# Kernel optimization log

Hardware: AMD Instinct MI355X
Metric: run time of the kernel (lower is better)

Reference implementation:

```python
import jax, jax.numpy as jnp
import numpy as np

NUM_PROPOSALS = 200000
NUM_OBJECTS = 128
N_CLS = 256
POS_THR = 0.4
NEG_THR = 0.1
REG_FACTOR = 10.0


def _make_boxes(key, n, img=1000.0, max_wh=200.0):
    k1, k2 = jax.random.split(key)
    xy = jax.random.uniform(k1, (n, 2), jnp.float32) * (img - max_wh)
    wh = jax.random.uniform(k2, (n, 2), jnp.float32) * (max_wh - 1.0) + 1.0
    return jnp.concatenate([xy, xy + wh], axis=-1)  # valid xyxy boxes


def setup_inputs() -> dict:
    key = jax.random.key(0)
    k1, k2, k3 = jax.random.split(key, 3)
    return {
        "objectness_score": jax.random.normal(k1, (NUM_PROPOSALS,), jnp.float32),
        "proposals": _make_boxes(k2, NUM_PROPOSALS),
        "gt_bounding_box": _make_boxes(k3, NUM_OBJECTS)[None],  # (1, N, 4)
    }


def _box_iou(b1, b2):
    # b1: (N,4), b2: (M,4) in xyxy -> (N, M)
    a1 = (b1[:, 2] - b1[:, 0]) * (b1[:, 3] - b1[:, 1])
    a2 = (b2[:, 2] - b2[:, 0]) * (b2[:, 3] - b2[:, 1])
    lt = jnp.maximum(b1[:, None, :2], b2[None, :, :2])
    rb = jnp.minimum(b1[:, None, 2:], b2[None, :, 2:])
    wh = jnp.clip(rb - lt, 0.0)
    inter = wh[..., 0] * wh[..., 1]
    return inter / (a1[:, None] + a2[None, :] - inter)


def _rpn_loss(objectness_score, proposals, gt_bounding_box):
    gt = gt_bounding_box[0]                      # (N, 4)
    iou = _box_iou(gt, proposals)                # (N, M)
    N, M = iou.shape
    flat = iou.reshape(-1)                       # (N*M,)

    # top-N best (gt, proposal) pairs, indices only (non-differentiable path)
    _, best_idx = jax.lax.top_k(flat, N)

    key = jax.random.key(42)
    k1, k2, k3 = jax.random.split(key, 3)
    neg_inf = jnp.float32(-jnp.inf)

    # random-priority sampling == randperm + truncate over candidate multiset
    pos_prio = jnp.where(flat > POS_THR, jax.random.uniform(k1, (N * M,)), neg_inf)
    best_prio = jax.random.uniform(k2, (N,))
    cand_prio = jnp.concatenate([best_prio, pos_prio])
    cand_idx = jnp.concatenate([best_idx, jnp.arange(N * M)])

    num_pos = N_CLS // 2   # always filled: best_idx contributes N=128 candidates
    num_neg = N_CLS - num_pos

    sel_p, loc = jax.lax.top_k(cand_prio, num_pos)
    pos_flat = cand_idx[loc]
    pos_valid = jnp.isfinite(sel_p)
    pos_rows = pos_flat // M
    pos_cols = pos_flat % M

    neg_prio = jnp.where(flat < NEG_THR, jax.random.uniform(k3, (N * M,)), neg_inf)
    sel_n, neg_flat = jax.lax.top_k(neg_prio, num_neg)
    neg_valid = jnp.isfinite(sel_n)
    neg_cols = neg_flat % M

    # classification: BCE-with-logits, mean over valid samples
    logits = jnp.concatenate([objectness_score[pos_cols], objectness_score[neg_cols]])
    labels = jnp.concatenate([jnp.ones((num_pos,), jnp.float32), jnp.zeros((num_neg,), jnp.float32)])
    w = jnp.concatenate([pos_valid, neg_valid]).astype(jnp.float32)
    bce = jnp.maximum(logits, 0.0) - logits * labels + jnp.log1p(jnp.exp(-jnp.abs(logits)))
    cls_loss = jnp.sum(bce * w) / jnp.maximum(jnp.sum(w), 1.0)

    d = proposals[pos_cols] - gt[pos_rows]       # (num_pos, 4)
    ad = jnp.abs(d)
    sl1 = jnp.where(ad < 1.0, 0.5 * d * d, ad - 0.5)
    wp = pos_valid.astype(jnp.float32)[:, None]
    reg_loss = jnp.sum(sl1 * wp) / jnp.maximum(jnp.sum(wp) * 4.0, 1.0)

    return cls_loss + REG_FACTOR * reg_loss


def reference(objectness_score, proposals, gt_bounding_box):
    return _rpn_loss(objectness_score, proposals, gt_bounding_box)
```

## Files before the change

### kernel.cpp

```cpp
#include <hip/hip_runtime.h>
#include <stdint.h>

#pragma clang fp contract(off)

typedef unsigned long long u64;
typedef uint32_t u32;

#define M_PROP 200000u
#define N_GT   128u
#define NM     25600000u
#define GSPLIT 4u
#define GPART  32u

#define BCUT 8355840u
#define CCUT 8387584u
#define IB_POS 0x3ECCCCCDu

#define SHARDS 16u
#define SHARD_CAP 4096u
#define ACAP_SHARD 65536u
#define TOPA_CAP 8192u
#define COMP_CAP 8192u
#define ACAP_L 512u

#define CSLOT(i) counters[(u32)(i) * 256u]

__host__ __device__ inline void tf2x32(u32 k0, u32 k1, u32 x0, u32 x1,
                                       u32& o0, u32& o1) {
  u32 ks0 = k0, ks1 = k1, ks2 = k0 ^ k1 ^ 0x1BD11BDAu;
  x0 += ks0; x1 += ks1;
#define TF_R(r) { x0 += x1; x1 = (x1 << r) | (x1 >> (32 - r)); x1 ^= x0; }
  TF_R(13) TF_R(15) TF_R(26) TF_R(6)
  x0 += ks1; x1 += ks2 + 1u;
  TF_R(17) TF_R(29) TF_R(16) TF_R(24)
  x0 += ks2; x1 += ks0 + 2u;
  TF_R(13) TF_R(15) TF_R(26) TF_R(6)
  x0 += ks0; x1 += ks1 + 3u;
  TF_R(17) TF_R(29) TF_R(16) TF_R(24)
  x0 += ks1; x1 += ks2 + 4u;
  TF_R(13) TF_R(15) TF_R(26) TF_R(6)
  x0 += ks2; x1 += ks0 + 5u;
#undef TF_R
  o0 = x0; o1 = x1;
}

__device__ inline u32 jax_bits32(u32 ka, u32 kb, u32 idx) {
  u32 a, b; tf2x32(ka, kb, 0u, idx, a, b);
  return a ^ b;
}

static void jax_split3(u32& k1a, u32& k1b, u32& k2a, u32& k2b,
                       u32& k3a, u32& k3b) {
  const u32 K0 = 0u, K1 = 42u;
  tf2x32(K0, K1, 0u, 0u, k1a, k1b);
  tf2x32(K0, K1, 0u, 1u, k2a, k2b);
  tf2x32(K0, K1, 0u, 2u, k3a, k3b);
}

__device__ inline u32 wave_append_slot(u32* ctr, bool pred, bool& any) {
  u64 mask = __ballot(pred);
  if (mask == 0ull) { any = false; return 0u; }
  any = true;
  u32 lane = threadIdx.x & 63u;
  u32 prefix = (u32)__popcll(mask & ((1ull << lane) - 1ull));
  int leader = __ffsll(mask) - 1;
  u32 base = 0u;
  if ((int)lane == leader) base = atomicAdd(ctr, (u32)__popcll(mask));
  base = __shfl(base, leader, 64);
  return base + prefix;
}

__device__ inline void wave_append4(u32* ctr, u64* buf, u32 cap,
                                    const bool* p, const u64* v) {
  u64 m0 = __ballot(p[0]);
  u64 m1 = __ballot(p[1]);
  u64 m2 = __ballot(p[2]);
  u64 m3 = __ballot(p[3]);
  u32 lane = threadIdx.x & 63u;
  u64 laneLT = (1ull << lane) - 1ull;
  u32 n0 = (u32)__popcll(m0), n1 = (u32)__popcll(m1);
  u32 n2 = (u32)__popcll(m2), n3 = (u32)__popcll(m3);
  int leader = __ffsll(m0 | m1 | m2 | m3) - 1;
  u32 base = 0u;
  if ((int)lane == leader) base = atomicAdd(ctr, n0 + n1 + n2 + n3);
  base = __shfl(base, leader, 64);
  if (p[0]) { u32 s = base + (u32)__popcll(m0 & laneLT); if (s < cap) buf[s] = v[0]; }
  base += n0;
  if (p[1]) { u32 s = base + (u32)__popcll(m1 & laneLT); if (s < cap) buf[s] = v[1]; }
  base += n1;
  if (p[2]) { u32 s = base + (u32)__popcll(m2 & laneLT); if (s < cap) buf[s] = v[2]; }
  base += n2;
  if (p[3]) { u32 s = base + (u32)__popcll(m3 & laneLT); if (s < cap) buf[s] = v[3]; }
}

__device__ inline u32 iouBin(u32 bits) {
  u32 b = (bits - 0x3E800000u) >> 14;
  return b > 1023u ? 1023u : b;
}

__global__ __launch_bounds__(256) void rpn_collect(
    const float4* __restrict__ props, const float4* __restrict__ gt,
    u64* __restrict__ bufA, u64* __restrict__ bufB, u64* __restrict__ bufC,
    u32* __restrict__ counters, u32* __restrict__ gHistA,
    u32 k1a, u32 k1b, u32 k3a, u32 k3b) {
  __shared__ float4 gtS[GPART];
  __shared__ float gtAreaS[GPART];
  __shared__ u32 hA[1024];
  __shared__ u64 listA[4][ACAP_L];
  const u32 tid = threadIdx.x;
  const u32 lane = tid & 63u;
  const u32 wid = tid >> 6;
  const u32 gbase = blockIdx.y * GPART;
  for (u32 i = tid; i < 1024u; i += 256u) hA[i] = 0u;
  for (u32 j = tid; j < GPART; j += 256u) {
    float4 gb = gt[gbase + j];
    gtS[j] = gb;
    gtAreaS[j] = (gb.z - gb.x) * (gb.w - gb.y);
  }
  __syncthreads();

  const u32 shard = (blockIdx.x * GSPLIT + blockIdx.y) & (SHARDS - 1u);
  u32* cntC_g = &CSLOT(shard);
  u32* cntB_g = &CSLOT(16u + shard);
  u32* cntA_g = &CSLOT(32u + shard);
  u64* myBufC = bufC + (size_t)shard * SHARD_CAP;
  u64* myBufB = bufB + (size_t)shard * SHARD_CAP;
  u64* myBufA = bufA + (size_t)shard * ACAP_SHARD;

  u32 p = blockIdx.x * 256u + tid;
  bool active = p < M_PROP;
  float4 pb = make_float4(0.f, 0.f, 0.f, 0.f);
  if (active) pb = props[p];
  float pa = (pb.z - pb.x) * (pb.w - pb.y);

  u32 cntA = 0u;
  const u64 laneLT = (1ull << lane) - 1ull;

#define PROCESS_A()                                                          \
  {                                                                          \
    for (u32 i = lane; i < cntA; i += 64u) {                                 \
      u64 kv = listA[wid][i];                                                \
      bool anyk;                                                             \
      u32 sk = wave_append_slot(cntA_g, true, anyk);                         \
      if (sk < ACAP_SHARD) myBufA[sk] = kv;                                  \
      u32 ib = (u32)(kv >> 25);                                              \
      u32 bidx = 0x1FFFFFFu - (u32)(kv & 0x1FFFFFFu);                        \
      u32 m1 = jax_bits32(k1a, k1b, bidx) >> 9;                              \
      bool keep = (ib > IB_POS) && (m1 >= BCUT);                             \
      bool anyb;                                                             \
      u32 sb2 = wave_append_slot(cntB_g, keep, anyb);                        \
      if (keep && sb2 < SHARD_CAP)                                           \
        myBufB[sb2] = ((u64)m1 << 25) | (u64)(0x1FFFFFFu - (bidx + 128u));   \
    }                                                                        \
    cntA = 0u;                                                               \
  }

  u32 idxRun = gbase * M_PROP + p;
  for (u32 gg = 0u; gg < GPART; gg += 4u) {
    float iou[4]; u32 ib[4], idx[4], m3[4];
    bool aa[4], cc[4];
#pragma unroll
    for (u32 r = 0u; r < 4u; ++r) {
      float4 gb = gtS[gg + r];
      float ga = gtAreaS[gg + r];
      float wx = fminf(gb.z, pb.z) - fmaxf(gb.x, pb.x);
      float wy = fminf(gb.w, pb.w) - fmaxf(gb.y, pb.y);
      wx = fmaxf(wx, 0.0f); wy = fmaxf(wy, 0.0f);
      float inter = wx * wy;
      iou[r] = inter / (ga + pa - inter);
      ib[r] = __float_as_uint(iou[r]);
      idx[r] = idxRun; idxRun += M_PROP;
      m3[r] = jax_bits32(k3a, k3b, idx[r]) >> 9;
      aa[r] = active && (iou[r] > 0.25f);
      cc[r] = active && (iou[r] < 0.1f) && (m3[r] >= CCUT);
      if (aa[r]) atomicAdd(&hA[iouBin(ib[r])], 1u);
    }
#pragma unroll
    for (u32 r = 0u; r < 4u; ++r) {
      u64 ma = __ballot(aa[r]);
      if (ma) {
        u32 pfx = (u32)__popcll(ma & laneLT);
        if (aa[r])
          listA[wid][cntA + pfx] = ((u64)ib[r] << 25) | (u64)(0x1FFFFFFu - idx[r]);
        cntA += (u32)__popcll(ma);
      }
    }
    u64 mc = __ballot(cc[0] | cc[1] | cc[2] | cc[3]);
    if (mc) {
      u64 cv[4];
#pragma unroll
      for (u32 r = 0u; r < 4u; ++r)
        cv[r] = ((u64)m3[r] << 25) | (u64)(0x1FFFFFFu - idx[r]);
      wave_append4(cntC_g, myBufC, SHARD_CAP, cc, cv);
    }
    if (cntA > ACAP_L - 256u) PROCESS_A();
  }
  PROCESS_A();
#undef PROCESS_A

  __syncthreads();
  for (u32 b = tid; b < 1024u; b += 256u) {
    u32 v = hA[b];
    if (v) atomicAdd(&gHistA[b], v);
  }
}

__global__ __launch_bounds__(256) void rpn_filterA(
    const u64* __restrict__ bufA, const u32* __restrict__ gHistA,
    u32* __restrict__ counters, u64* __restrict__ bufTopA) {
  const u32 tid = threadIdx.x;
  const u32 lane = tid & 63u;
  u32 loc[16]; u32 t = 0u;
  const u32 bbase = lane * 16u;
#pragma unroll
  for (u32 j = 0u; j < 16u; ++j) { loc[j] = gHistA[bbase + j]; t += loc[j]; }
  u32 suf = t;
  for (u32 off = 1u; off < 64u; off <<= 1u) {
    u32 o = __shfl_down(suf, off, 64);
    if (lane + off < 64u) suf += o;
  }
  u32 cum = suf - t;
  u32 cand = 0u; bool found = false;
#pragma unroll
  for (int j = 15; j >= 0; --j) {
    cum += loc[j];
    if (!found && cum >= 128u) { cand = bbase + (u32)j; found = true; }
  }
  for (u32 off = 1u; off < 64u; off <<= 1u) {
    u32 o = __shfl_xor(cand, off, 64);
    cand = o > cand ? o : cand;
  }
  const u32 cut = cand;
  for (u32 sh = 0u; sh < SHARDS; ++sh) {
    u32 n = CSLOT(32u + sh); n = n < ACAP_SHARD ? n : ACAP_SHARD;
    const u64* sb = bufA + (size_t)sh * ACAP_SHARD;
    for (u32 i = blockIdx.x * 256u + tid; i < n; i += gridDim.x * 256u) {
      u64 k = sb[i];
      bool keep = iouBin((u32)(k >> 25)) >= cut;
      bool any;
      u32 s = wave_append_slot(&CSLOT(48), keep, any);
      if (keep && s < TOPA_CAP) bufTopA[s] = k;
    }
  }
}

__device__ inline void rank_select(const u64* cand, u32 nc, u64* selKey) {
  const u32 tid = threadIdx.x;
  if (tid < 128u) selKey[tid] = 0ull;
  u64 k[8]; u32 r[8];
#pragma unroll
  for (int j = 0; j < 8; ++j) {
    u32 i = tid + (u32)j * 1024u;
    k[j] = (i < nc) ? cand[i] : 0ull;
    r[j] = 0u;
  }
  __syncthreads();
  for (u32 i = 0u; i < nc; ++i) {
    u64 v = cand[i];
#pragma unroll
    for (int j = 0; j < 8; ++j) r[j] += (v > k[j]) ? 1u : 0u;
  }
#pragma unroll
  for (int j = 0; j < 8; ++j) {
    u32 i = tid + (u32)j * 1024u;
    if (i < nc && r[j] < 128u) selKey[r[j]] = k[j];
  }
  __syncthreads();
}

__device__ inline void rank_select2(const u64* cand, u32 nc, u64* selKey) {
  const u32 tid = threadIdx.x;
  if (tid < 128u) selKey[tid] = 0ull;
  u64 mine = (tid < nc) ? cand[tid] : 0ull;
  __syncthreads();
  u32 r = 0u;
  for (u32 i = 0u; i < nc; ++i) r += (cand[i] > mine) ? 1u : 0u;
  if (tid < nc && r < 128u) selKey[r] = mine;
  __syncthreads();
}

__device__ inline float sl1(float d) {
  float ad = fabsf(d);
  return (ad < 1.0f) ? 0.5f * d * d : ad - 0.5f;
}

__global__ __launch_bounds__(1024) void rpn_finalize(
    const float* __restrict__ obj, const float4* __restrict__ props,
    const float4* __restrict__ gt,
    const u64* __restrict__ bufTopA,
    const u64* __restrict__ bufB, const u64* __restrict__ bufC,
    const u32* __restrict__ counters, float* __restrict__ out,
    u32 k2a, u32 k2b) {
  __shared__ u64 keyBuf[COMP_CAP];
  __shared__ u64 keyBuf2[1024];
  __shared__ u64 selKey[128];
  __shared__ u32 bestIdx[128];
  __shared__ u32 hist64[64];
  __shared__ float pr[16];
  __shared__ u32 s_cnt, s_cnt2, s_cutLo;
  __shared__ float s_reg, s_bcep;

  const u32 tid = threadIdx.x;
  const u32 lane = tid & 63u;
  const u32 wid = tid >> 6u;

  u32 nT = CSLOT(48); nT = nT < TOPA_CAP ? nT : TOPA_CAP;
  for (u32 i = tid; i < nT; i += 1024u) keyBuf[i] = bufTopA[i];
  __syncthreads();
  if (nT <= 1024u) rank_select2(keyBuf, nT, selKey);
  else rank_select(keyBuf, nT, selKey);
  if (tid < 128u) {
    u64 k = selKey[tid];
    bestIdx[tid] = (k == 0ull) ? 0u : (0x1FFFFFFu - (u32)(k & 0x1FFFFFFu));
  }
  __syncthreads();

  if (tid == 0u) { s_cnt = 128u; s_cnt2 = 0u; }
  if (tid < 64u) hist64[tid] = 0u;
  __syncthreads();
  if (tid < 128u) {
    u32 m2 = jax_bits32(k2a, k2b, tid) >> 9;
    keyBuf[tid] = ((u64)m2 << 25) | (u64)(0x1FFFFFFu - tid);
    if (m2 >= BCUT) atomicAdd(&hist64[(m2 - BCUT) >> 9], 1u);
  }
  {
    u32 n = CSLOT(16u + wid); n = n < SHARD_CAP ? n : SHARD_CAP;
    const u64* sb = bufB + (size_t)wid * SHARD_CAP;
    for (u32 i = lane; i < n; i += 64u) {
      u64 k = sb[i];
      bool any;
      u32 s = wave_append_slot(&s_cnt, true, any);
      if (s < COMP_CAP) keyBuf[s] = k;
      atomicAdd(&hist64[((u32)(k >> 25) - BCUT) >> 9], 1u);
    }
  }
  __syncthreads();
  u32 nc = s_cnt < COMP_CAP ? s_cnt : COMP_CAP;
  if (wid == 0u) {
    u32 suf = hist64[lane];
    for (u32 off = 1u; off < 64u; off <<= 1u) {
      u32 o = __shfl_down(suf, off, 64);
      if (lane + off < 64u) suf += o;
    }
    u64 ok = __ballot(suf >= 128u);
    u32 cutLo = 0u;
    if (ok) cutLo = BCUT + ((63u - (u32)__clzll(ok)) << 9);
    if (lane == 0u) s_cutLo = cutLo;
  }
  __syncthreads();
  {
    u64 cutKey = ((u64)s_cutLo) << 25;
    for (u32 i = tid; i < nc; i += 1024u) {
      u64 k = keyBuf[i];
      if (k >= cutKey) {
        u32 s = atomicAdd(&s_cnt2, 1u);
        if (s < 1024u) keyBuf2[s] = k;
      }
    }
  }
  __syncthreads();
  u32 ns = s_cnt2;
  if (ns <= 1024u) rank_select2(keyBuf2, ns, selKey);
  else rank_select(keyBuf, nc, selKey);

  float locReg = 0.0f, locBce = 0.0f;
  if (tid < 128u) {
    u64 k = selKey[tid];
    if (k != 0ull) {
      u32 c = 0x1FFFFFFu - (u32)(k & 0x1FFFFFFu);
      u32 pair = (c < 128u) ? bestIdx[c] : (c - 128u);
      if (pair < NM) {
        u32 row = pair / M_PROP, col = pair % M_PROP;
        float4 prb = props[col];
        float4 gb = gt[row];
        locReg = sl1(prb.x - gb.x) + sl1(prb.y - gb.y) +
                 sl1(prb.z - gb.z) + sl1(prb.w - gb.w);
        float l = obj[col];
        locBce = fmaxf(l, 0.0f) - l + log1pf(expf(-fabsf(l)));
      }
    }
  }
  {
    float v = locReg;
    for (u32 off = 32u; off > 0u; off >>= 1u) v += __shfl_xor(v, off, 64);
    if (lane == 0u) pr[wid] = v;
    __syncthreads();
    if (tid == 0u) {
      float s = 0.0f;
#pragma unroll
      for (u32 w = 0u; w < 16u; ++w) s += pr[w];
      s_reg = s;
    }
    __syncthreads();
    v = locBce;
    for (u32 off = 32u; off > 0u; off >>= 1u) v += __shfl_xor(v, off, 64);
    if (lane == 0u) pr[wid] = v;
    __syncthreads();
    if (tid == 0u) {
      float s = 0.0f;
#pragma unroll
      for (u32 w = 0u; w < 16u; ++w) s += pr[w];
      s_bcep = s;
    }
    __syncthreads();
  }

  if (tid == 0u) { s_cnt = 0u; s_cnt2 = 0u; }
  if (tid < 64u) hist64[tid] = 0u;
  __syncthreads();
  {
    u32 n = CSLOT(wid); n = n < SHARD_CAP ? n : SHARD_CAP;
    const u64* sb = bufC + (size_t)wid * SHARD_CAP;
    for (u32 i = lane; i < n; i += 64u) {
      u64 k = sb[i];
      bool any;
      u32 s = wave_append_slot(&s_cnt, true, any);
      if (s < COMP_CAP) keyBuf[s] = k;
      atomicAdd(&hist64[((u32)(k >> 25) - CCUT) >> 4], 1u);
    }
  }
  __syncthreads();
  nc = s_cnt < COMP_CAP ? s_cnt : COMP_CAP;
  if (wid == 0u) {
    u32 suf = hist64[lane];
    for (u32 off = 1u; off < 64u; off <<= 1u) {
      u32 o = __shfl_down(suf, off, 64);
      if (lane + off < 64u) suf += o;
    }
    u64 ok = __ballot(suf >= 128u);
    u32 cutLo = 0u;
    if (ok) cutLo = CCUT + ((63u - (u32)__clzll(ok)) << 4);
    if (lane == 0u) s_cutLo = cutLo;
  }
  __syncthreads();
  {
    u64 cutKey = ((u64)s_cutLo) << 25;
    for (u32 i = tid; i < nc; i += 1024u) {
      u64 k = keyBuf[i];
      if (k >= cutKey) {
        u32 s = atomicAdd(&s_cnt2, 1u);
        if (s < 1024u) keyBuf2[s] = k;
      }
    }
  }
  __syncthreads();
  ns = s_cnt2;
  if (ns <= 1024u) rank_select2(keyBuf2, ns, selKey);
  else rank_select(keyBuf, nc, selKey);

  float locBceN = 0.0f;
  if (tid < 128u) {
    u64 k = selKey[tid];
    if (k != 0ull) {
      u32 idx = 0x1FFFFFFu - (u32)(k & 0x1FFFFFFu);
      u32 col = idx % M_PROP;
      float l = obj[col];
      locBceN = fmaxf(l, 0.0f) + log1pf(expf(-fabsf(l)));
    }
  }
  {
    float v = locBceN;
    for (u32 off = 32u; off > 0u; off >>= 1u) v += __shfl_xor(v, off, 64);
    if (lane == 0u) pr[wid] = v;
    __syncthreads();
    if (tid == 0u) {
      float s = 0.0f;
#pragma unroll
      for (u32 w = 0u; w < 16u; ++w) s += pr[w];
      float cls = (s_bcep + s) / 256.0f;
      float reg = s_reg / 512.0f;
      out[0] = cls + 10.0f * reg;
    }
  }
}

extern "C" void kernel_launch(void* const* d_in, const int* in_sizes, int n_in,
                              void* d_out, int out_size, void* d_ws, size_t ws_size,
                              hipStream_t stream) {
  (void)in_sizes; (void)n_in; (void)out_size; (void)ws_size;
  const float* obj = (const float*)d_in[0];
  const float4* props = (const float4*)d_in[1];
  const float4* gt = (const float4*)d_in[2];
  float* out = (float*)d_out;

  u32 k1a, k1b, k2a, k2b, k3a, k3b;
  jax_split3(k1a, k1b, k2a, k2b, k3a, k3b);

  uint8_t* base = (uint8_t*)d_ws;
  u32* counters = (u32*)base;
  u32* gHistA = (u32*)(base + 65536);
  u64* bufTopA = (u64*)(base + 65536 + 4096);
  u64* bufB = (u64*)(base + 65536 + 4096 + (size_t)TOPA_CAP * 8);
  u64* bufC = bufB + (size_t)SHARDS * SHARD_CAP;
  u64* bufA = bufC + (size_t)SHARDS * SHARD_CAP;

  const u32 gridX = (M_PROP + 255u) / 256u;
  hipMemsetAsync(d_ws, 0, 65536 + 4096, stream);
  rpn_collect<<<dim3(gridX, GSPLIT), 256, 0, stream>>>(
      props, gt, bufA, bufB, bufC, counters, gHistA, k1a, k1b, k3a, k3b);
  rpn_filterA<<<64, 256, 0, stream>>>(bufA, gHistA, counters, bufTopA);
  rpn_finalize<<<1, 1024, 0, stream>>>(obj, props, gt, bufTopA, bufB, bufC,
                                       counters, out, k2a, k2b);
}
```

Measured before the change: 112.0 us.

## Defer IoU divisions to candidate paths and shrink shared candidate list

The main loop no longer computes an IoU division for every pair. It pre-filters A candidates with a multiply-based comparison (inter > 0.2499*union), computes the exact division only for the rare C candidates that pass the random cut, and recomputes the exact IoU (re-reading the proposal) for A-list entries in the flush path. The shared A list now stores 32-bit indices instead of 64-bit keys, which halves LDS use. It also uses a hardware rotate in threefry and mbcnt for lane prefixes. In exchange, the flush path does extra global loads and divisions, and the 0.2499 margin must be conservative enough that the exact filter still matches the original.

New measurement: 107.9 us. 3.7% less time.

```diff
diff --git a/kernel.cpp b/kernel.cpp
--- a/kernel.cpp
+++ b/kernel.cpp
@@ -25,11 +25,22 @@
 
 #define CSLOT(i) counters[(u32)(i) * 256u]
 
+__device__ inline u32 rotl32(u32 x, u32 r) { return __builtin_rotateleft32(x, r); }
+
+__device__ inline u32 lane_prefix(u64 mask) {
+  return __builtin_amdgcn_mbcnt_hi((u32)(mask >> 32),
+                                   __builtin_amdgcn_mbcnt_lo((u32)mask, 0u));
+}
+
 __host__ __device__ inline void tf2x32(u32 k0, u32 k1, u32 x0, u32 x1,
                                        u32& o0, u32& o1) {
   u32 ks0 = k0, ks1 = k1, ks2 = k0 ^ k1 ^ 0x1BD11BDAu;
   x0 += ks0; x1 += ks1;
+#ifdef __HIP_DEVICE_COMPILE__
+#define TF_R(r) { x0 += x1; x1 = rotl32(x1, r); x1 ^= x0; }
+#else
 #define TF_R(r) { x0 += x1; x1 = (x1 << r) | (x1 >> (32 - r)); x1 ^= x0; }
+#endif
   TF_R(13) TF_R(15) TF_R(26) TF_R(6)
   x0 += ks1; x1 += ks2 + 1u;
   TF_R(17) TF_R(29) TF_R(16) TF_R(24)
@@ -61,11 +72,11 @@
   u64 mask = __ballot(pred);
   if (mask == 0ull) { any = false; return 0u; }
   any = true;
-  u32 lane = threadIdx.x & 63u;
-  u32 prefix = (u32)__popcll(mask & ((1ull << lane) - 1ull));
+  u32 prefix = lane_prefix(mask);
   int leader = __ffsll(mask) - 1;
   u32 base = 0u;
-  if ((int)lane == leader) base = atomicAdd(ctr, (u32)__popcll(mask));
+  if ((int)(threadIdx.x & 63u) == leader)
+    base = atomicAdd(ctr, (u32)__popcll(mask));
   base = __shfl(base, leader, 64);
   return base + prefix;
 }
@@ -76,21 +87,20 @@
   u64 m1 = __ballot(p[1]);
   u64 m2 = __ballot(p[2]);
   u64 m3 = __ballot(p[3]);
-  u32 lane = threadIdx.x & 63u;
-  u64 laneLT = (1ull << lane) - 1ull;
   u32 n0 = (u32)__popcll(m0), n1 = (u32)__popcll(m1);
   u32 n2 = (u32)__popcll(m2), n3 = (u32)__popcll(m3);
   int leader = __ffsll(m0 | m1 | m2 | m3) - 1;
   u32 base = 0u;
-  if ((int)lane == leader) base = atomicAdd(ctr, n0 + n1 + n2 + n3);
+  if ((int)(threadIdx.x & 63u) == leader)
+    base = atomicAdd(ctr, n0 + n1 + n2 + n3);
   base = __shfl(base, leader, 64);
-  if (p[0]) { u32 s = base + (u32)__popcll(m0 & laneLT); if (s < cap) buf[s] = v[0]; }
+  if (p[0]) { u32 s = base + lane_prefix(m0); if (s < cap) buf[s] = v[0]; }
   base += n0;
-  if (p[1]) { u32 s = base + (u32)__popcll(m1 & laneLT); if (s < cap) buf[s] = v[1]; }
+  if (p[1]) { u32 s = base + lane_prefix(m1); if (s < cap) buf[s] = v[1]; }
   base += n1;
-  if (p[2]) { u32 s = base + (u32)__popcll(m2 & laneLT); if (s < cap) buf[s] = v[2]; }
+  if (p[2]) { u32 s = base + lane_prefix(m2); if (s < cap) buf[s] = v[2]; }
   base += n2;
-  if (p[3]) { u32 s = base + (u32)__popcll(m3 & laneLT); if (s < cap) buf[s] = v[3]; }
+  if (p[3]) { u32 s = base + lane_prefix(m3); if (s < cap) buf[s] = v[3]; }
 }
 
 __device__ inline u32 iouBin(u32 bits) {
@@ -106,7 +116,7 @@
   __shared__ float4 gtS[GPART];
   __shared__ float gtAreaS[GPART];
   __shared__ u32 hA[1024];
-  __shared__ u64 listA[4][ACAP_L];
+  __shared__ u32 listA[4][ACAP_L];
   const u32 tid = threadIdx.x;
   const u32 lane = tid & 63u;
   const u32 wid = tid >> 6;
@@ -134,31 +144,43 @@
   float pa = (pb.z - pb.x) * (pb.w - pb.y);
 
   u32 cntA = 0u;
-  const u64 laneLT = (1ull << lane) - 1ull;
 
 #define PROCESS_A()                                                          \
   {                                                                          \
     for (u32 i = lane; i < cntA; i += 64u) {                                 \
-      u64 kv = listA[wid][i];                                                \
+      u32 aidx = listA[wid][i];                                              \
+      u32 row = aidx / M_PROP;                                               \
+      u32 col = aidx - row * M_PROP;                                         \
+      float4 pbx = props[col];                                               \
+      float4 gbx = gtS[row - gbase];                                         \
+      float gax = gtAreaS[row - gbase];                                      \
+      float pax = (pbx.z - pbx.x) * (pbx.w - pbx.y);                         \
+      float wxx = fminf(gbx.z, pbx.z) - fmaxf(gbx.x, pbx.x);                 \
+      float wyy = fminf(gbx.w, pbx.w) - fmaxf(gbx.y, pbx.y);                 \
+      wxx = fmaxf(wxx, 0.0f); wyy = fmaxf(wyy, 0.0f);                        \
+      float interx = wxx * wyy;                                              \
+      float ioux = interx / (gax + pax - interx);                            \
+      u32 ib = __float_as_uint(ioux);                                        \
+      bool isA = ioux > 0.25f;                                               \
+      if (isA) atomicAdd(&hA[iouBin(ib)], 1u);                               \
       bool anyk;                                                             \
-      u32 sk = wave_append_slot(cntA_g, true, anyk);                         \
-      if (sk < ACAP_SHARD) myBufA[sk] = kv;                                  \
-      u32 ib = (u32)(kv >> 25);                                              \
-      u32 bidx = 0x1FFFFFFu - (u32)(kv & 0x1FFFFFFu);                        \
-      u32 m1 = jax_bits32(k1a, k1b, bidx) >> 9;                              \
-      bool keep = (ib > IB_POS) && (m1 >= BCUT);                             \
+      u32 sk = wave_append_slot(cntA_g, isA, anyk);                          \
+      if (isA && sk < ACAP_SHARD)                                            \
+        myBufA[sk] = ((u64)ib << 25) | (u64)(0x1FFFFFFu - aidx);             \
+      u32 m1 = jax_bits32(k1a, k1b, aidx) >> 9;                              \
+      bool keep = isA && (ib > IB_POS) && (m1 >= BCUT);                      \
       bool anyb;                                                             \
       u32 sb2 = wave_append_slot(cntB_g, keep, anyb);                        \
       if (keep && sb2 < SHARD_CAP)                                           \
-        myBufB[sb2] = ((u64)m1 << 25) | (u64)(0x1FFFFFFu - (bidx + 128u));   \
+        myBufB[sb2] = ((u64)m1 << 25) | (u64)(0x1FFFFFFu - (aidx + 128u));   \
     }                                                                        \
     cntA = 0u;                                                               \
   }
 
   u32 idxRun = gbase * M_PROP + p;
   for (u32 gg = 0u; gg < GPART; gg += 4u) {
-    float iou[4]; u32 ib[4], idx[4], m3[4];
-    bool aa[4], cc[4];
+    float inter[4], uni[4]; u32 idx[4], m3[4];
+    bool aa[4], ccp[4];
 #pragma unroll
     for (u32 r = 0u; r < 4u; ++r) {
       float4 gb = gtS[gg + r];
@@ -166,31 +188,31 @@
       float wx = fminf(gb.z, pb.z) - fmaxf(gb.x, pb.x);
       float wy = fminf(gb.w, pb.w) - fmaxf(gb.y, pb.y);
       wx = fmaxf(wx, 0.0f); wy = fmaxf(wy, 0.0f);
-      float inter = wx * wy;
-      iou[r] = inter / (ga + pa - inter);
-      ib[r] = __float_as_uint(iou[r]);
+      inter[r] = wx * wy;
+      uni[r] = ga + pa - inter[r];
       idx[r] = idxRun; idxRun += M_PROP;
       m3[r] = jax_bits32(k3a, k3b, idx[r]) >> 9;
-      aa[r] = active && (iou[r] > 0.25f);
-      cc[r] = active && (iou[r] < 0.1f) && (m3[r] >= CCUT);
-      if (aa[r]) atomicAdd(&hA[iouBin(ib[r])], 1u);
+      aa[r] = active && (inter[r] > 0.2499f * uni[r]);
+      ccp[r] = active && (m3[r] >= CCUT);
     }
 #pragma unroll
     for (u32 r = 0u; r < 4u; ++r) {
       u64 ma = __ballot(aa[r]);
       if (ma) {
-        u32 pfx = (u32)__popcll(ma & laneLT);
-        if (aa[r])
-          listA[wid][cntA + pfx] = ((u64)ib[r] << 25) | (u64)(0x1FFFFFFu - idx[r]);
+        u32 pfx = lane_prefix(ma);
+        if (aa[r]) listA[wid][cntA + pfx] = idx[r];
         cntA += (u32)__popcll(ma);
       }
     }
-    u64 mc = __ballot(cc[0] | cc[1] | cc[2] | cc[3]);
+    u64 mc = __ballot(ccp[0] | ccp[1] | ccp[2] | ccp[3]);
     if (mc) {
-      u64 cv[4];
-#pragma unroll
-      for (u32 r = 0u; r < 4u; ++r)
+      bool cc[4]; u64 cv[4];
+#pragma unroll
+      for (u32 r = 0u; r < 4u; ++r) {
+        float iouX = inter[r] / uni[r];
+        cc[r] = ccp[r] && (iouX < 0.1f);
         cv[r] = ((u64)m3[r] << 25) | (u64)(0x1FFFFFFu - idx[r]);
+      }
       wave_append4(cntC_g, myBufC, SHARD_CAP, cc, cv);
     }
     if (cntA > ACAP_L - 256u) PROCESS_A();
```
